# Kernel optimization log

Hardware: AMD Instinct MI355X
Metric: run time of the kernel (lower is better)

## Reference

```python
import jax, jax.numpy as jnp
import numpy as np

N_NODES = 100000
N_EDGES = 819200
D = 512
L = 3
LN_EPS = 1e-5


def setup_inputs() -> dict:
    key = jax.random.key(0)
    ks = jax.random.split(key, 8)
    x = jax.random.normal(ks[0], (N_NODES, D), dtype=jnp.float32)
    edge_index = jax.random.randint(ks[1], (2, N_EDGES), 0, N_NODES, dtype=jnp.int32)
    scale = 1.0 / np.sqrt(D)
    W_l = jax.random.normal(ks[2], (L, D, D), dtype=jnp.float32) * scale  # neighbor transform
    W_r = jax.random.normal(ks[3], (L, D, D), dtype=jnp.float32) * scale  # root transform
    b = jax.random.normal(ks[4], (L, D), dtype=jnp.float32) * 0.01
    ln_g = jnp.ones((L, D), dtype=jnp.float32)
    ln_b = jnp.zeros((L, D), dtype=jnp.float32)
    return {"x": x, "edge_index": edge_index, "W_l": W_l, "W_r": W_r,
            "b": b, "ln_g": ln_g, "ln_b": ln_b}


def reference(x, edge_index, W_l, W_r, b, ln_g, ln_b):
    # SAGEConv (mean aggr) x L layers, each followed by LayerNorm, ReLU,
    # dropout (p=0, identity in eval) and residual add. batch=None -> node embeddings.
    src = edge_index[0]  # message sources (x_j)
    tgt = edge_index[1]  # aggregation targets (x_i)
    n = x.shape[0]
    cnt = jax.ops.segment_sum(jnp.ones((src.shape[0],), x.dtype), tgt, num_segments=n)
    inv_cnt = (1.0 / jnp.maximum(cnt, 1.0))[:, None]  # mean; isolated nodes -> 0
    for i in range(W_l.shape[0]):
        x_in = x
        agg = jax.ops.segment_sum(x[src], tgt, num_segments=n) * inv_cnt  # [N, D]
        h = agg @ W_l[i].T + x @ W_r[i].T + b[i]
        mu = jnp.mean(h, axis=-1, keepdims=True)
        var = jnp.mean(jnp.square(h - mu), axis=-1, keepdims=True)
        h = (h - mu) * jax.lax.rsqrt(var + LN_EPS) * ln_g[i] + ln_b[i]
        h = jax.nn.relu(h)
        x = h + x_in  # residual (shapes always match: D==D)
    return x
```

## Files before the change

### kernel.cpp

```cpp
#include <hip/hip_runtime.h>
#include <hip/hip_bf16.h>
#include <cstdint>

#define N_NODES 100000
#define N_EDGES 819200
#define D 512
#define LAYERS 3
#define LN_EPS 1e-5f

typedef __bf16 bf16x8 __attribute__((ext_vector_type(8)));
typedef float floatx4 __attribute__((ext_vector_type(4)));

__device__ __forceinline__ void bf2x2(uint32_t u, float& lo, float& hi) {
    union { uint32_t i; float f; } a, b;
    a.i = u << 16; b.i = u & 0xFFFF0000u;
    lo = a.f; hi = b.f;
}
__device__ __forceinline__ uint16_t f2bf(float f) {
    union { float f; uint32_t i; } v; v.f = f;
    uint32_t r = v.i + 0x7FFFu + ((v.i >> 16) & 1u);
    return (uint16_t)(r >> 16);
}
__device__ __forceinline__ uint32_t f2bf2(float lo, float hi) {
    return (uint32_t)f2bf(lo) | ((uint32_t)f2bf(hi) << 16);
}

__device__ __forceinline__ void async16(const uint16_t* g, uint16_t* lds) {
    __builtin_amdgcn_global_load_lds(
        (const __attribute__((address_space(1))) uint32_t*)g,
        (__attribute__((address_space(3))) uint32_t*)lds, 16, 0, 0);
}

__global__ void k_count(const int* __restrict__ tgt, int* __restrict__ cnt) {
    int e = blockIdx.x * blockDim.x + threadIdx.x;
    if (e < N_EDGES) atomicAdd(&cnt[tgt[e]], 1);
}

__global__ void k_scan(const int* __restrict__ cnt, int* __restrict__ row_start,
                       int* __restrict__ cursor) {
    __shared__ int wsum[16];
    const int t = threadIdx.x;
    const int lane = t & 63, wid = t >> 6;
    int running = 0;
    for (int base = 0; base < N_NODES; base += 1024) {
        int idx = base + t;
        int v = (idx < N_NODES) ? cnt[idx] : 0;
        int x = v;
        #pragma unroll
        for (int off = 1; off < 64; off <<= 1) {
            int n = __shfl_up(x, off, 64);
            if (lane >= off) x += n;
        }
        if (lane == 63) wsum[wid] = x;
        __syncthreads();
        if (wid == 0) {
            int s = (lane < 16) ? wsum[lane] : 0;
            #pragma unroll
            for (int off = 1; off < 16; off <<= 1) {
                int n = __shfl_up(s, off, 64);
                if (lane >= off) s += n;
            }
            if (lane < 16) wsum[lane] = s;
        }
        __syncthreads();
        int waveoff = (wid > 0) ? wsum[wid - 1] : 0;
        int excl = running + x + waveoff - v;
        if (idx < N_NODES) { row_start[idx] = excl; cursor[idx] = excl; }
        int chunk_total = wsum[15];
        __syncthreads();
        running += chunk_total;
    }
    if (t == 0) row_start[N_NODES] = running;
}

__global__ void k_scatter(const int* __restrict__ src, const int* __restrict__ tgt,
                          int* __restrict__ cursor, int* __restrict__ src_sorted) {
    int e = blockIdx.x * blockDim.x + threadIdx.x;
    if (e < N_EDGES) {
        int p = atomicAdd(&cursor[tgt[e]], 1);
        src_sorted[p] = src[e];
    }
}

__global__ void k_f2bf(const float* __restrict__ in, uint16_t* __restrict__ out, int n) {
    int i = (blockIdx.x * blockDim.x + threadIdx.x) * 8;
    if (i < n) {
        float4 a = *(const float4*)(in + i);
        float4 b = *(const float4*)(in + i + 4);
        uint4 o;
        o.x = f2bf2(a.x, a.y); o.y = f2bf2(a.z, a.w);
        o.z = f2bf2(b.x, b.y); o.w = f2bf2(b.z, b.w);
        *(uint4*)(out + i) = o;
    }
}

__global__ void k_wcat(const float* __restrict__ Wl, const float* __restrict__ Wr,
                       uint16_t* __restrict__ wcat) {
    int i = blockIdx.x * blockDim.x + threadIdx.x;
    int k = i & 1023;
    int j = (i >> 10) & 511;
    int l = i >> 19;
    float v = (k < 512) ? Wl[((size_t)l * 512 + j) * 512 + k]
                        : Wr[((size_t)l * 512 + j) * 512 + (k - 512)];
    wcat[i] = f2bf(v);
}

__device__ __forceinline__ void agg_acc(float* acc, uint4 p) {
    float lo, hi;
    bf2x2(p.x, lo, hi); acc[0] += lo; acc[1] += hi;
    bf2x2(p.y, lo, hi); acc[2] += lo; acc[3] += hi;
    bf2x2(p.z, lo, hi); acc[4] += lo; acc[5] += hi;
    bf2x2(p.w, lo, hi); acc[6] += lo; acc[7] += hi;
}

__global__ __launch_bounds__(256)
void k_agg(const uint16_t* __restrict__ x_bf, const int* __restrict__ row_start,
           const int* __restrict__ src_sorted, uint16_t* __restrict__ agg_bf) {
    const int wid = threadIdx.x >> 6, lane = threadIdx.x & 63;
    const int node = blockIdx.x * 4 + wid;
    if (node >= N_NODES) return;
    const int s0 = row_start[node], s1 = row_start[node + 1];
    const int col = lane * 8;
    float acc[8] = {0.f, 0.f, 0.f, 0.f, 0.f, 0.f, 0.f, 0.f};
    int e = s0;
    for (; e + 4 <= s1; e += 4) {
        int i0 = src_sorted[e], i1 = src_sorted[e + 1];
        int i2 = src_sorted[e + 2], i3 = src_sorted[e + 3];
        uint4 p0 = *(const uint4*)(x_bf + (size_t)i0 * D + col);
        uint4 p1 = *(const uint4*)(x_bf + (size_t)i1 * D + col);
        uint4 p2 = *(const uint4*)(x_bf + (size_t)i2 * D + col);
        uint4 p3 = *(const uint4*)(x_bf + (size_t)i3 * D + col);
        agg_acc(acc, p0); agg_acc(acc, p1); agg_acc(acc, p2); agg_acc(acc, p3);
    }
    if (e + 2 <= s1) {
        int i0 = src_sorted[e], i1 = src_sorted[e + 1];
        uint4 p0 = *(const uint4*)(x_bf + (size_t)i0 * D + col);
        uint4 p1 = *(const uint4*)(x_bf + (size_t)i1 * D + col);
        agg_acc(acc, p0); agg_acc(acc, p1);
        e += 2;
    }
    if (e < s1) {
        int i0 = src_sorted[e];
        uint4 p0 = *(const uint4*)(x_bf + (size_t)i0 * D + col);
        agg_acc(acc, p0);
    }
    const float inv = (s1 > s0) ? 1.0f / (float)(s1 - s0) : 0.0f;
    uint4 o;
    o.x = f2bf2(acc[0] * inv, acc[1] * inv);
    o.y = f2bf2(acc[2] * inv, acc[3] * inv);
    o.z = f2bf2(acc[4] * inv, acc[5] * inv);
    o.w = f2bf2(acc[6] * inv, acc[7] * inv);
    *(uint4*)(agg_bf + (size_t)node * D + col) = o;
}

__device__ __forceinline__ int lds_sw(int r, int q) { return r * 32 + (((q + r) & 3) << 3); }

__global__ __launch_bounds__(256)
void k_gemm(const uint16_t* __restrict__ A0,
            const uint16_t* __restrict__ A1,
            const uint16_t* __restrict__ W,
            uint16_t* __restrict__ Hout)
{
    __shared__ uint16_t Als[128 * 32];
    __shared__ uint16_t Wls[128 * 32];
    const int tid = threadIdx.x;
    const int lane = tid & 63, wid = tid >> 6;
    const int wm = wid >> 1, wn = wid & 1;
    const int rb = blockIdx.x >> 2, cb = blockIdx.x & 3;
    const int row0 = rb * 128, col0 = cb * 128;

    const int lr = lane >> 2, qs = lane & 3;
    const int rc0 = wid * 32 + lr;
    const int rc1 = wid * 32 + 16 + lr;
    const int q0 = (qs - rc0) & 3;
    const int q1 = (qs - rc1) & 3;
    int gr0 = row0 + rc0; if (gr0 > N_NODES - 1) gr0 = N_NODES - 1;
    int gr1 = row0 + rc1; if (gr1 > N_NODES - 1) gr1 = N_NODES - 1;
    const size_t woff0 = (size_t)(col0 + rc0) * 1024 + q0 * 8;
    const size_t woff1 = (size_t)(col0 + rc1) * 1024 + q1 * 8;
    uint16_t* ldsA0 = &Als[(wid * 32) * 32];
    uint16_t* ldsA1 = &Als[(wid * 32 + 16) * 32];
    uint16_t* ldsW0 = &Wls[(wid * 32) * 32];
    uint16_t* ldsW1 = &Wls[(wid * 32 + 16) * 32];

    const int m = lane & 15;
    const int qm = lane >> 4;

    floatx4 acc[4][4] = {};

    for (int kb = 0; kb < 1024; kb += 32) {
        const uint16_t* Ab; int kl;
        if (kb < 512) { Ab = A0; kl = kb; } else { Ab = A1; kl = kb - 512; }
        async16(Ab + (size_t)gr0 * 512 + kl + q0 * 8, ldsA0);
        async16(Ab + (size_t)gr1 * 512 + kl + q1 * 8, ldsA1);
        async16(W + woff0 + kb, ldsW0);
        async16(W + woff1 + kb, ldsW1);
        __syncthreads();

        bf16x8 af[4], bfr[4];
        #pragma unroll
        for (int mt = 0; mt < 4; mt++)
            af[mt] = *(bf16x8*)&Als[lds_sw(wm * 64 + mt * 16 + m, qm)];
        #pragma unroll
        for (int nt = 0; nt < 4; nt++)
            bfr[nt] = *(bf16x8*)&Wls[lds_sw(wn * 64 + nt * 16 + m, qm)];
        #pragma unroll
        for (int mt = 0; mt < 4; mt++)
            #pragma unroll
            for (int nt = 0; nt < 4; nt++)
                acc[mt][nt] = __builtin_amdgcn_mfma_f32_16x16x32_bf16(
                    af[mt], bfr[nt], acc[mt][nt], 0, 0, 0);
        __syncthreads();
    }

    #pragma unroll
    for (int mt = 0; mt < 4; mt++) {
        #pragma unroll
        for (int r = 0; r < 4; r++) {
            int grow = row0 + wm * 64 + mt * 16 + qm * 4 + r;
            if (grow < N_NODES) {
                #pragma unroll
                for (int nt = 0; nt < 4; nt++) {
                    int gcol = col0 + wn * 64 + nt * 16 + m;
                    Hout[(size_t)grow * 512 + gcol] = f2bf(acc[mt][nt][r]);
                }
            }
        }
    }
}

__global__ __launch_bounds__(256)
void k_ln(const uint16_t* __restrict__ H, const float* __restrict__ bias,
          const float* __restrict__ gam, const float* __restrict__ bet,
          uint16_t* __restrict__ xbf,
          float* __restrict__ out32, int last) {
    const int wid = threadIdx.x >> 6, lane = threadIdx.x & 63;
    const int node = blockIdx.x * 4 + wid;
    if (node >= N_NODES) return;
    const int col = lane * 8;
    const size_t off = (size_t)node * D + col;

    uint4 hp = *(const uint4*)(H + off);
    float v[8];
    bf2x2(hp.x, v[0], v[1]); bf2x2(hp.y, v[2], v[3]);
    bf2x2(hp.z, v[4], v[5]); bf2x2(hp.w, v[6], v[7]);
    float4 b0 = *(const float4*)(bias + col), b1 = *(const float4*)(bias + col + 4);
    v[0] += b0.x; v[1] += b0.y; v[2] += b0.z; v[3] += b0.w;
    v[4] += b1.x; v[5] += b1.y; v[6] += b1.z; v[7] += b1.w;

    float s = 0.f;
    #pragma unroll
    for (int i = 0; i < 8; i++) s += v[i];
    #pragma unroll
    for (int o = 32; o >= 1; o >>= 1) s += __shfl_xor(s, o, 64);
    float mu = s * (1.0f / D);
    float vs = 0.f;
    #pragma unroll
    for (int i = 0; i < 8; i++) { float d = v[i] - mu; vs += d * d; }
    #pragma unroll
    for (int o = 32; o >= 1; o >>= 1) vs += __shfl_xor(vs, o, 64);
    float rstd = rsqrtf(vs * (1.0f / D) + LN_EPS);

    float4 g0 = *(const float4*)(gam + col), g1 = *(const float4*)(gam + col + 4);
    float4 e0 = *(const float4*)(bet + col), e1 = *(const float4*)(bet + col + 4);
    float gg[8] = {g0.x, g0.y, g0.z, g0.w, g1.x, g1.y, g1.z, g1.w};
    float ee[8] = {e0.x, e0.y, e0.z, e0.w, e1.x, e1.y, e1.z, e1.w};

    uint4 xp = *(const uint4*)(xbf + off);
    float xi[8];
    bf2x2(xp.x, xi[0], xi[1]); bf2x2(xp.y, xi[2], xi[3]);
    bf2x2(xp.z, xi[4], xi[5]); bf2x2(xp.w, xi[6], xi[7]);

    float o_[8];
    #pragma unroll
    for (int i = 0; i < 8; i++) {
        float h = (v[i] - mu) * rstd * gg[i] + ee[i];
        o_[i] = fmaxf(h, 0.f) + xi[i];
    }
    if (last) {
        float4 f0 = {o_[0], o_[1], o_[2], o_[3]};
        float4 f1 = {o_[4], o_[5], o_[6], o_[7]};
        *(float4*)(out32 + off) = f0;
        *(float4*)(out32 + off + 4) = f1;
    } else {
        uint4 o;
        o.x = f2bf2(o_[0], o_[1]); o.y = f2bf2(o_[2], o_[3]);
        o.z = f2bf2(o_[4], o_[5]); o.w = f2bf2(o_[6], o_[7]);
        *(uint4*)(xbf + off) = o;
    }
}

extern "C" void kernel_launch(void* const* d_in, const int* in_sizes, int n_in,
                              void* d_out, int out_size, void* d_ws, size_t ws_size,
                              hipStream_t stream) {
    const float* x   = (const float*)d_in[0];
    const int*   ei  = (const int*)d_in[1];
    const float* Wl  = (const float*)d_in[2];
    const float* Wr  = (const float*)d_in[3];
    const float* b   = (const float*)d_in[4];
    const float* g   = (const float*)d_in[5];
    const float* be  = (const float*)d_in[6];
    float* out = (float*)d_out;
    const int* src = ei;
    const int* tgt = ei + N_EDGES;

    size_t off = 0;
    auto alloc = [&](size_t bytes) -> void* {
        void* p = (char*)d_ws + off;
        off += (bytes + 255) & ~(size_t)255;
        return p;
    };
    int* cnt        = (int*)alloc((size_t)N_NODES * 4);
    int* row_start  = (int*)alloc((size_t)(N_NODES + 1) * 4);
    int* cursor     = (int*)alloc((size_t)N_NODES * 4);
    int* src_sorted = (int*)alloc((size_t)N_EDGES * 4);
    uint16_t* wcat  = (uint16_t*)alloc((size_t)LAYERS * 512 * 1024 * 2);
    uint16_t* x_bf  = (uint16_t*)alloc((size_t)N_NODES * D * 2);
    uint16_t* agg_bf= (uint16_t*)alloc((size_t)N_NODES * D * 2);
    uint16_t* h_bf  = (uint16_t*)alloc((size_t)N_NODES * D * 2);

    (void)hipMemsetAsync(cnt, 0, (size_t)N_NODES * 4, stream);
    k_count<<<N_EDGES / 256, 256, 0, stream>>>(tgt, cnt);
    k_scan<<<1, 1024, 0, stream>>>(cnt, row_start, cursor);
    k_scatter<<<N_EDGES / 256, 256, 0, stream>>>(src, tgt, cursor, src_sorted);
    k_f2bf<<<(N_NODES * D / 8) / 256, 256, 0, stream>>>(x, x_bf, N_NODES * D);
    k_wcat<<<(LAYERS * 512 * 1024) / 256, 256, 0, stream>>>(Wl, Wr, wcat);

    const int gemm_grid = ((N_NODES + 127) / 128) * 4;
    for (int l = 0; l < LAYERS; l++) {
        k_agg<<<N_NODES / 4, 256, 0, stream>>>(x_bf, row_start, src_sorted, agg_bf);
        k_gemm<<<gemm_grid, 256, 0, stream>>>(agg_bf, x_bf,
                                              wcat + (size_t)l * 512 * 1024, h_bf);
        k_ln<<<N_NODES / 4, 256, 0, stream>>>(h_bf, b + l * D, g + l * D, be + l * D,
                                              x_bf, out, l == 2 ? 1 : 0);
    }
}
```

Measured before the change: 1.530 ms.

## Rewrite GEMM as 256x256 tile, double-buffered LDS with XCD-aware block remap

The GEMM moves from a 128x128 tile with a single LDS buffer and a full barrier on every K step to a 256x256 tile computed by 512 threads. A, B loads are double-buffered asynchronously with explicit vmcnt waits, and reads from LDS are interleaved with MFMA quads under s_setprio. Block IDs are remapped so consecutive tiles land on the same XCD, and LDS uses an XOR swizzle. This targets better data reuse, hiding load latency behind MFMA, and L2 locality. In exchange it uses much more LDS and registers (one block per CU) and depends on hand-counted wait counts that are fragile.

```diff
diff --git a/kernel.cpp b/kernel.cpp
--- a/kernel.cpp
+++ b/kernel.cpp
@@ -8,6 +8,8 @@
 #define LAYERS 3
 #define LN_EPS 1e-5f
 
+#define GEMM_GRID 782
+
 typedef __bf16 bf16x8 __attribute__((ext_vector_type(8)));
 typedef float floatx4 __attribute__((ext_vector_type(4)));
 
@@ -30,6 +32,12 @@
         (const __attribute__((address_space(1))) uint32_t*)g,
         (__attribute__((address_space(3))) uint32_t*)lds, 16, 0, 0);
 }
+
+#define BARRIER() do { asm volatile("" ::: "memory"); \
+                       __builtin_amdgcn_s_barrier();   \
+                       asm volatile("" ::: "memory"); } while (0)
+#define VMCNT6() asm volatile("s_waitcnt vmcnt(6)" ::: "memory")
+#define VMCNT0() asm volatile("s_waitcnt vmcnt(0)" ::: "memory")
 
 __global__ void k_count(const int* __restrict__ tgt, int* __restrict__ cnt) {
     int e = blockIdx.x * blockDim.x + threadIdx.x;
@@ -153,76 +161,138 @@
     *(uint4*)(agg_bf + (size_t)node * D + col) = o;
 }
 
-__device__ __forceinline__ int lds_sw(int r, int q) { return r * 32 + (((q + r) & 3) << 3); }
-
-__global__ __launch_bounds__(256)
+__global__ __launch_bounds__(512, 1)
 void k_gemm(const uint16_t* __restrict__ A0,
             const uint16_t* __restrict__ A1,
             const uint16_t* __restrict__ W,
             uint16_t* __restrict__ Hout)
 {
-    __shared__ uint16_t Als[128 * 32];
-    __shared__ uint16_t Wls[128 * 32];
+    __shared__ uint16_t Ash0[256 * 64];
+    __shared__ uint16_t Ash1[256 * 64];
+    __shared__ uint16_t Bsh0[256 * 64];
+    __shared__ uint16_t Bsh1[256 * 64];
+
     const int tid = threadIdx.x;
-    const int lane = tid & 63, wid = tid >> 6;
-    const int wm = wid >> 1, wn = wid & 1;
-    const int rb = blockIdx.x >> 2, cb = blockIdx.x & 3;
-    const int row0 = rb * 128, col0 = cb * 128;
-
-    const int lr = lane >> 2, qs = lane & 3;
-    const int rc0 = wid * 32 + lr;
-    const int rc1 = wid * 32 + 16 + lr;
-    const int q0 = (qs - rc0) & 3;
-    const int q1 = (qs - rc1) & 3;
-    int gr0 = row0 + rc0; if (gr0 > N_NODES - 1) gr0 = N_NODES - 1;
-    int gr1 = row0 + rc1; if (gr1 > N_NODES - 1) gr1 = N_NODES - 1;
-    const size_t woff0 = (size_t)(col0 + rc0) * 1024 + q0 * 8;
-    const size_t woff1 = (size_t)(col0 + rc1) * 1024 + q1 * 8;
-    uint16_t* ldsA0 = &Als[(wid * 32) * 32];
-    uint16_t* ldsA1 = &Als[(wid * 32 + 16) * 32];
-    uint16_t* ldsW0 = &Wls[(wid * 32) * 32];
-    uint16_t* ldsW1 = &Wls[(wid * 32 + 16) * 32];
-
-    const int m = lane & 15;
-    const int qm = lane >> 4;
-
-    floatx4 acc[4][4] = {};
-
-    for (int kb = 0; kb < 1024; kb += 32) {
-        const uint16_t* Ab; int kl;
-        if (kb < 512) { Ab = A0; kl = kb; } else { Ab = A1; kl = kb - 512; }
-        async16(Ab + (size_t)gr0 * 512 + kl + q0 * 8, ldsA0);
-        async16(Ab + (size_t)gr1 * 512 + kl + q1 * 8, ldsA1);
-        async16(W + woff0 + kb, ldsW0);
-        async16(W + woff1 + kb, ldsW1);
-        __syncthreads();
-
-        bf16x8 af[4], bfr[4];
-        #pragma unroll
-        for (int mt = 0; mt < 4; mt++)
-            af[mt] = *(bf16x8*)&Als[lds_sw(wm * 64 + mt * 16 + m, qm)];
-        #pragma unroll
-        for (int nt = 0; nt < 4; nt++)
-            bfr[nt] = *(bf16x8*)&Wls[lds_sw(wn * 64 + nt * 16 + m, qm)];
-        #pragma unroll
-        for (int mt = 0; mt < 4; mt++)
+    const int l = tid & 63, w = tid >> 6;
+    const int wm = w >> 2, wn = w & 3;
+    const int wmA = wm * 128, wnB = wn * 64;
+    const int mrow = l & 15, qbase = l >> 4, sw7 = l & 7;
+
+    const int bid = blockIdx.x;
+    const int xcd = bid & 7, pos = bid >> 3;
+    const int wk = (xcd < 6 ? xcd * 98 : 588 + (xcd - 6) * 97) + pos;
+    const int rb = wk >> 1, cb = wk & 1;
+    const int row0 = rb * 256, col0 = cb * 256;
+
+    const int ra = w * 8 + (l >> 3);
+    const int o16 = (l & 7) ^ ((l >> 3) & 7);
+    uint32_t offA[2][2], offB[2][2];
+    #pragma unroll
+    for (int h = 0; h < 2; h++)
+        #pragma unroll
+        for (int j = 0; j < 2; j++) {
+            int rr = h * 128 + j * 64 + ra;
+            int gra = row0 + rr; if (gra > N_NODES - 1) gra = N_NODES - 1;
+            offA[h][j] = (uint32_t)gra * 1024u + (uint32_t)o16 * 16u;
+            offB[h][j] = (uint32_t)(col0 + rr) * 2048u + (uint32_t)o16 * 16u;
+        }
+
+    auto stA = [&](uint16_t* buf, int h, int t_) {
+        int ts = t_ < 15 ? t_ : 15;
+        const char* base; uint32_t koff;
+        if (ts < 8) { base = (const char*)A0; koff = (uint32_t)ts * 128u; }
+        else        { base = (const char*)A1; koff = (uint32_t)(ts - 8) * 128u; }
+        async16((const uint16_t*)(base + offA[h][0] + koff), buf + (h * 128 + w * 8) * 64);
+        async16((const uint16_t*)(base + offA[h][1] + koff), buf + (h * 128 + 64 + w * 8) * 64);
+    };
+    auto stB = [&](uint16_t* buf, int h, int t_) {
+        int ts = t_ < 15 ? t_ : 15;
+        uint32_t koff = (uint32_t)ts * 128u;
+        async16((const uint16_t*)((const char*)W + offB[h][0] + koff), buf + (h * 128 + w * 8) * 64);
+        async16((const uint16_t*)((const char*)W + offB[h][1] + koff), buf + (h * 128 + 64 + w * 8) * 64);
+    };
+
+    floatx4 acc[8][4] = {};
+    bf16x8 af[4][2], bA[2][2], bB[2][2];
+
+    auto rdA4 = [&](bf16x8 a_[4][2], const uint16_t* buf, int rbase) {
+        #pragma unroll
+        for (int mr = 0; mr < 4; mr++) {
+            int r = wmA + rbase + mr * 16 + mrow;
             #pragma unroll
-            for (int nt = 0; nt < 4; nt++)
-                acc[mt][nt] = __builtin_amdgcn_mfma_f32_16x16x32_bf16(
-                    af[mt], bfr[nt], acc[mt][nt], 0, 0, 0);
-        __syncthreads();
-    }
-
-    #pragma unroll
-    for (int mt = 0; mt < 4; mt++) {
-        #pragma unroll
-        for (int r = 0; r < 4; r++) {
-            int grow = row0 + wm * 64 + mt * 16 + qm * 4 + r;
+            for (int kh = 0; kh < 2; kh++) {
+                int slot = (kh * 4 + qbase) ^ sw7;
+                a_[mr][kh] = *(const bf16x8*)(buf + r * 64 + slot * 8);
+            }
+        }
+    };
+    auto rdB2 = [&](bf16x8 b_[2][2], const uint16_t* buf, int nbase) {
+        #pragma unroll
+        for (int nr = 0; nr < 2; nr++) {
+            int r = wnB + (nbase + nr) * 16 + mrow;
+            #pragma unroll
+            for (int kh = 0; kh < 2; kh++) {
+                int slot = (kh * 4 + qbase) ^ sw7;
+                b_[nr][kh] = *(const bf16x8*)(buf + r * 64 + slot * 8);
+            }
+        }
+    };
+    auto quad = [&](const bf16x8 a_[4][2], const bf16x8 b_[2][2], int mb, int nb) {
+        __builtin_amdgcn_s_setprio(1);
+        #pragma unroll
+        for (int mr = 0; mr < 4; mr++)
+            #pragma unroll
+            for (int nr = 0; nr < 2; nr++)
+                #pragma unroll
+                for (int kh = 0; kh < 2; kh++)
+                    acc[mb + mr][nb + nr] = __builtin_amdgcn_mfma_f32_16x16x32_bf16(
+                        a_[mr][kh], b_[nr][kh], acc[mb + mr][nb + nr], 0, 0, 0);
+        __builtin_amdgcn_s_setprio(0);
+    };
+
+    stB(Bsh0, 0, 0); stB(Bsh0, 1, 0); stA(Ash0, 0, 0); stA(Ash0, 1, 0);
+    stB(Bsh1, 0, 1); stB(Bsh1, 1, 1); stA(Ash1, 0, 1);
+    VMCNT6();
+    BARRIER();
+
+    #pragma unroll 1
+    for (int i = 0; i < 8; i++) {
+        const int te = 2 * i, to = 2 * i + 1;
+        rdA4(af, Ash0, 0); rdB2(bA, Bsh0, 0);
+        stA(Ash1, 1, to);
+        BARRIER(); quad(af, bA, 0, 0); BARRIER();
+        rdB2(bB, Bsh0, 2);
+        BARRIER(); quad(af, bB, 0, 2); BARRIER();
+        rdA4(af, Ash0, 64);
+        stB(Bsh0, 0, te + 2); stB(Bsh0, 1, te + 2);
+        BARRIER(); quad(af, bA, 4, 0); BARRIER();
+        stA(Ash0, 0, te + 2);
+        VMCNT6();
+        BARRIER(); quad(af, bB, 4, 2); BARRIER();
+        rdA4(af, Ash1, 0); rdB2(bA, Bsh1, 0);
+        stA(Ash0, 1, te + 2);
+        BARRIER(); quad(af, bA, 0, 0); BARRIER();
+        rdB2(bB, Bsh1, 2);
+        BARRIER(); quad(af, bB, 0, 2); BARRIER();
+        rdA4(af, Ash1, 64);
+        stB(Bsh1, 0, to + 2); stB(Bsh1, 1, to + 2);
+        BARRIER(); quad(af, bA, 4, 0); BARRIER();
+        stA(Ash1, 0, to + 2);
+        VMCNT6();
+        BARRIER(); quad(af, bB, 4, 2); BARRIER();
+    }
+    VMCNT0();
+
+    #pragma unroll
+    for (int mr = 0; mr < 8; mr++) {
+        #pragma unroll
+        for (int rr = 0; rr < 4; rr++) {
+            int grow = row0 + wmA + mr * 16 + qbase * 4 + rr;
             if (grow < N_NODES) {
                 #pragma unroll
-                for (int nt = 0; nt < 4; nt++) {
-                    int gcol = col0 + wn * 64 + nt * 16 + m;
-                    Hout[(size_t)grow * 512 + gcol] = f2bf(acc[mt][nt][r]);
+                for (int nr = 0; nr < 4; nr++) {
+                    int gcol = col0 + wnB + nr * 16 + mrow;
+                    Hout[(size_t)grow * 512 + gcol] = f2bf(acc[mr][nr][rr]);
                 }
             }
         }
@@ -326,10 +396,9 @@
     k_f2bf<<<(N_NODES * D / 8) / 256, 256, 0, stream>>>(x, x_bf, N_NODES * D);
     k_wcat<<<(LAYERS * 512 * 1024) / 256, 256, 0, stream>>>(Wl, Wr, wcat);
 
-    const int gemm_grid = ((N_NODES + 127) / 128) * 4;
     for (int l = 0; l < LAYERS; l++) {
         k_agg<<<N_NODES / 4, 256, 0, stream>>>(x_bf, row_start, src_sorted, agg_bf);
-        k_gemm<<<gemm_grid, 256, 0, stream>>>(agg_bf, x_bf,
+        k_gemm<<<GEMM_GRID, 512, 0, stream>>>(agg_bf, x_bf,
                                               wcat + (size_t)l * 512 * 1024, h_bf);
         k_ln<<<N_NODES / 4, 256, 0, stream>>>(h_bf, b + l * D, g + l * D, be + l * D,
                                               x_bf, out, l == 2 ? 1 : 0);
```

Result: faster. 1.490 ms (-2.6%).
